# Kernel optimization log

Measured on AMD Instinct MI355X. Metric: run time of the kernel, lower is better.

The kernel has to match this reference:

```python
import jax, jax.numpy as jnp
import numpy as np

B, S, H, W, L = 32, 512, 768, 256, 8  # batch, subword seq, hidden, max words, max group size
INTENT, SLOT = 26, 121


def setup_inputs() -> dict:
    key = jax.random.key(0)
    ks = jax.random.split(key, 16)
    sc = 0.02
    res_all = jax.random.normal(ks[0], (B, S, H), jnp.float32)
    res = jax.random.normal(ks[1], (B, H), jnp.float32)
    # group covers indices start..start+lens inclusive (lens+1 <= L elements)
    token_start_idxs = jax.random.randint(ks[2], (B, W), 0, S - L, jnp.int32)
    subword_lengths = jax.random.randint(ks[3], (B, W), 1, L, jnp.int32)  # 1..7
    return {
        'res_all': res_all,
        'res': res,
        'token_start_idxs': token_start_idxs,
        'subword_lengths': subword_lengths,
        'Wsq_w': jax.random.normal(ks[4], (H, H), jnp.float32) * sc,
        'Wsq_b': jnp.zeros((H,), jnp.float32),
        'Wsk_w': jax.random.normal(ks[5], (H, H), jnp.float32) * sc,
        'Wsk_b': jnp.zeros((H,), jnp.float32),
        'Wsv_w': jax.random.normal(ks[6], (H, H), jnp.float32) * sc,
        'Wsv_b': jnp.zeros((H,), jnp.float32),
        'lin_id_w': jax.random.normal(ks[7], (INTENT, H), jnp.float32) * sc,
        'lin_id_b': jnp.zeros((INTENT,), jnp.float32),
        'lin_slot_w': jax.random.normal(ks[8], (SLOT, H), jnp.float32) * sc,
        'lin_slot_b': jnp.zeros((SLOT,), jnp.float32),
    }


def reference(res_all, res, token_start_idxs, subword_lengths,
              Wsq_w, Wsq_b, Wsk_w, Wsk_b, Wsv_w, Wsv_b,
              lin_id_w, lin_id_b, lin_slot_w, lin_slot_b):
    # intent head on pooled output
    res_id = res @ lin_id_w.T + lin_id_b  # [B, INTENT]

    # gather padded subword groups: torch.range is inclusive -> lens+1 subwords
    offs = jnp.arange(L, dtype=jnp.int32)                        # [L]
    idx = token_start_idxs[:, :, None] + offs[None, None, :]     # [B, W, L]
    idx = jnp.clip(idx, 0, S - 1)
    group = res_all[jnp.arange(B)[:, None, None], idx]           # [B, W, L, H]
    valid = offs[None, None, :] <= subword_lengths[:, :, None]   # [B, W, L], lens+1 valid

    # SAA_Attn: only the first row's attention output is used
    q0 = group[:, :, 0, :] @ Wsq_w.T + Wsq_b                     # [B, W, H]
    K = group @ Wsk_w.T + Wsk_b                                  # [B, W, L, H]
    V = group @ Wsv_w.T + Wsv_b                                  # [B, W, L, H]
    scores = jnp.einsum('bwh,bwkh->bwk', q0, K)                  # [B, W, L]
    scores = jnp.where(valid, scores, jnp.float32(-1e9))
    attn = jax.nn.softmax(scores, axis=-1)
    first = group[:, :, 0, :]
    attn_word = jnp.einsum('bwk,bwkh->bwh', attn, V) + first     # [B, W, H]

    # lens == 1 branch bypasses attention entirely
    word = jnp.where((subword_lengths == 1)[:, :, None], first, attn_word)

    res_sf = word @ lin_slot_w.T + lin_slot_b                    # [B, W, SLOT]
    return res_id, res_sf
```

## Files before the change

### kernel.cpp

```cpp
#include <hip/hip_runtime.h>
#include <cstdint>
#include <cstddef>

#define BB 32
#define SS 512
#define HH 768
#define WW 256
#define LL 8
#define NINTENT 26
#define NSLOT 121

typedef float f32x4 __attribute__((ext_vector_type(4)));
typedef __bf16 bf16x8 __attribute__((ext_vector_type(8)));

static __device__ __forceinline__ float bf2f(unsigned short u) {
    union { unsigned int i; float f; } x; x.i = ((unsigned int)u) << 16; return x.f;
}
static __device__ __forceinline__ unsigned short f2bf(float f) {
    union { float f; unsigned int i; } x; x.f = f;
    unsigned int r = (x.i + 0x7fffu + ((x.i >> 16) & 1u)) >> 16;
    return (unsigned short)r;
}

static __device__ __forceinline__ void gload16(const void* g, void* l) {
    __builtin_amdgcn_global_load_lds(
        (const __attribute__((address_space(1))) void*)g,
        (__attribute__((address_space(3))) void*)l, 16, 0, 0);
}

#define MF(a, b, c) __builtin_amdgcn_mfma_f32_16x16x32_bf16((a), (b), (c), 0, 0, 0)

__global__ __launch_bounds__(256) void prep_w(
    const float* __restrict__ Wk, const float* __restrict__ Wq,
    const float* __restrict__ Wv, const float* __restrict__ Ws,
    const float* __restrict__ bq, const float* __restrict__ bv,
    unsigned short* __restrict__ WkT_hi, unsigned short* __restrict__ WkT_lo,
    unsigned short* __restrict__ WqT_hi, unsigned short* __restrict__ WqT_lo,
    unsigned short* __restrict__ WvT, unsigned short* __restrict__ Wcomb,
    float* __restrict__ u_part,
    float* __restrict__ wsbv_part)
{
    int bid = blockIdx.x;
    int t = threadIdx.x;

    if (bid < 432) {
        __shared__ float tl[64][65];
        int mb = bid / 144, tb = bid % 144;
        int tx = tb % 12, ty = tb / 12;
        const float* src = (mb == 0) ? Wk : (mb == 1) ? Wq : Wv;
        int rr = t >> 4, c4 = (t & 15) * 4;
#pragma unroll
        for (int j = 0; j < 4; j++) {
            float4 v = *reinterpret_cast<const float4*>(
                &src[(size_t)(ty * 64 + rr + 16 * j) * HH + tx * 64 + c4]);
            tl[rr + 16 * j][c4 + 0] = v.x; tl[rr + 16 * j][c4 + 1] = v.y;
            tl[rr + 16 * j][c4 + 2] = v.z; tl[rr + 16 * j][c4 + 3] = v.w;
        }
        __syncthreads();
        int il = t >> 4, o4 = (t & 15) * 4;
        unsigned short* dhi = (mb == 0) ? WkT_hi : (mb == 1) ? WqT_hi : WvT;
        unsigned short* dlo = (mb == 0) ? WkT_lo : WqT_lo;
#pragma unroll
        for (int j = 0; j < 4; j++) {
            int i = il + 16 * j;
            float v0 = tl[o4 + 0][i], v1 = tl[o4 + 1][i];
            float v2 = tl[o4 + 2][i], v3 = tl[o4 + 3][i];
            size_t off = (size_t)(tx * 64 + i) * HH + ty * 64 + o4;
            ushort4 h;
            h.x = f2bf(v0); h.y = f2bf(v1); h.z = f2bf(v2); h.w = f2bf(v3);
            *reinterpret_cast<ushort4*>(&dhi[off]) = h;
            if (mb < 2) {
                ushort4 l;
                l.x = f2bf(v0 - bf2f(h.x)); l.y = f2bf(v1 - bf2f(h.y));
                l.z = f2bf(v2 - bf2f(h.z)); l.w = f2bf(v3 - bf2f(h.w));
                *reinterpret_cast<ushort4*>(&dlo[off]) = l;
            }
        }
        if (mb == 0) {
            int c = t >> 2, q = t & 3;
            float s = 0.f;
#pragma unroll
            for (int r = 0; r < 16; r++)
                s += bq[ty * 64 + q * 16 + r] * tl[q * 16 + r][c];
            s += __shfl_xor(s, 1);
            s += __shfl_xor(s, 2);
            if (q == 0) u_part[ty * HH + tx * 64 + c] = s;
        }
    } else {
        __shared__ float wred[4];
        int bid2 = bid - 432;
        int idx = bid2 * 256 + t;
        int row = idx / HH, col = idx % HH;
        float v = (row < NSLOT) ? Ws[row * HH + col] : 0.f;
        Wcomb[row * 1536 + col] = f2bf(v);
        float pv = v * bv[col];
        int lane = t & 63, wave = t >> 6;
#pragma unroll
        for (int off = 32; off > 0; off >>= 1) pv += __shfl_xor(pv, off);
        if (lane == 0) wred[wave] = pv;
        __syncthreads();
        if (t == 0)
            wsbv_part[(bid2 % 3) * 128 + row] = wred[0] + wred[1] + wred[2] + wred[3];
    }
}

__global__ __launch_bounds__(256) void gemm_weights(
    const uint4* __restrict__ WkT_hi, const uint4* __restrict__ WkT_lo,
    const uint4* __restrict__ WqT_hi, const uint4* __restrict__ WqT_lo,
    const uint4* __restrict__ WvT, const uint4* __restrict__ Wcomb,
    const float* __restrict__ res_all, const int* __restrict__ starts,
    const float* __restrict__ res, const float* __restrict__ id_w,
    const float* __restrict__ id_b,
    float* __restrict__ Ppart,
    float* __restrict__ WRpart,
    unsigned short* __restrict__ slotA,
    float* __restrict__ out)
{
    __shared__ uint4 sA[512];
    __shared__ uint4 sB[512];
    int bid = blockIdx.x;
    int t = threadIdx.x;
    int lane = t & 63, wave = t >> 6;

    if (bid >= 2384) {
        int w = (bid - 2384) * 4 + wave;
        int bb = w / 26, o = w - bb * 26;
        const float* rrow = res + bb * HH + lane * 12;
        const float* wrow = id_w + o * HH + lane * 12;
        float s = 0.f;
#pragma unroll
        for (int c = 0; c < 3; c++) {
            float4 a = *reinterpret_cast<const float4*>(&rrow[c * 4]);
            float4 b = *reinterpret_cast<const float4*>(&wrow[c * 4]);
            s += a.x * b.x + a.y * b.y + a.z * b.z + a.w * b.w;
        }
#pragma unroll
        for (int off = 32; off > 0; off >>= 1) s += __shfl_xor(s, off);
        if (lane == 0) out[bb * NINTENT + o] = s + id_b[o];
        return;
    }
    if (bid >= 336) {
        int gw = (bid - 336) * 4 + wave;
        int b = gw >> 8;
        int s0 = starts[gw];
        const float* src = res_all + (size_t)(b * SS + s0) * HH + lane * 12;
        unsigned short* dst = slotA + (size_t)gw * 1536 + lane * 12;
#pragma unroll
        for (int c2 = 0; c2 < 3; c2++) {
            float4 v = *reinterpret_cast<const float4*>(&src[c2 * 4]);
            ushort4 o;
            o.x = f2bf(v.x); o.y = f2bf(v.y); o.z = f2bf(v.z); o.w = f2bf(v.w);
            *reinterpret_cast<ushort4*>(&dst[c2 * 4]) = o;
        }
        return;
    }

    int wm = wave >> 1, wn = wave & 1;
    int l16 = lane & 15, lk = lane >> 4;
    int srow = lane >> 2, schk = lane & 3;
    uint4* sA0 = &sA[wave * 128];
    uint4* sA1 = &sA[wave * 128 + 64];
    uint4* sB0 = &sB[wave * 128];
    uint4* sB1 = &sB[wave * 128 + 64];

    f32x4 acc[4][4] = {};

    if (bid < 288) {
        int tile = bid >> 3, ks = bid & 7;
        int mt = tile / 6, nt = tile % 6;
        int kb = ks * 12;
#pragma unroll
        for (int p = 0; p < 3; p++) {
            const uint4* Ab = (p == 1) ? WkT_lo : WkT_hi;
            const uint4* Bb = (p == 2) ? WqT_lo : WqT_hi;
            const uint4* Ag0 = Ab + (size_t)(mt * 128 + wave * 32 + srow) * 96 + kb + schk;
            const uint4* Ag1 = Ag0 + (size_t)16 * 96;
            const uint4* Bg0 = Bb + (size_t)(nt * 128 + wave * 32 + srow) * 96 + kb + schk;
            const uint4* Bg1 = Bg0 + (size_t)16 * 96;
            for (int k0 = 0; k0 < 12; k0 += 4) {
                gload16(Ag0 + k0, sA0); gload16(Ag1 + k0, sA1);
                gload16(Bg0 + k0, sB0); gload16(Bg1 + k0, sB1);
                __syncthreads();
                bf16x8 af[4], bfr[4];
#pragma unroll
                for (int i = 0; i < 4; i++)
                    af[i] = *reinterpret_cast<const bf16x8*>(&sA[(wm * 64 + i * 16 + l16) * 4 + lk]);
#pragma unroll
                for (int j = 0; j < 4; j++)
                    bfr[j] = *reinterpret_cast<const bf16x8*>(&sB[(wn * 64 + j * 16 + l16) * 4 + lk]);
#pragma unroll
                for (int i = 0; i < 4; i++)
#pragma unroll
                    for (int j = 0; j < 4; j++)
                        acc[i][j] = MF(af[i], bfr[j], acc[i][j]);
                __syncthreads();
            }
        }
        float* dst = Ppart + (size_t)ks * 589824;
#pragma unroll
        for (int i = 0; i < 4; i++)
#pragma unroll
            for (int j = 0; j < 4; j++) {
                int col = nt * 128 + wn * 64 + j * 16 + l16;
#pragma unroll
                for (int q = 0; q < 4; q++) {
                    int row = mt * 128 + wm * 64 + i * 16 + lk * 4 + q;
                    dst[(size_t)row * HH + col] = acc[i][j][q];
                }
            }
    } else {
        int idx = bid - 288;
        int nt = idx >> 3, ks = idx & 7;
        int kb = ks * 12;
        const uint4* Ag0 = Wcomb + (size_t)(wave * 32 + srow) * 192 + kb + schk;
        const uint4* Ag1 = Ag0 + (size_t)16 * 192;
        const uint4* Bg0 = WvT + (size_t)(nt * 128 + wave * 32 + srow) * 96 + kb + schk;
        const uint4* Bg1 = Bg0 + (size_t)16 * 96;
        for (int k0 = 0; k0 < 12; k0 += 4) {
            gload16(Ag0 + k0, sA0); gload16(Ag1 + k0, sA1);
            gload16(Bg0 + k0, sB0); gload16(Bg1 + k0, sB1);
            __syncthreads();
            bf16x8 af[4], bfr[4];
#pragma unroll
            for (int i = 0; i < 4; i++)
                af[i] = *reinterpret_cast<const bf16x8*>(&sA[(wm * 64 + i * 16 + l16) * 4 + lk]);
#pragma unroll
            for (int j = 0; j < 4; j++)
                bfr[j] = *reinterpret_cast<const bf16x8*>(&sB[(wn * 64 + j * 16 + l16) * 4 + lk]);
#pragma unroll
            for (int i = 0; i < 4; i++)
#pragma unroll
                for (int j = 0; j < 4; j++)
                    acc[i][j] = MF(af[i], bfr[j], acc[i][j]);
            __syncthreads();
        }
        float* dst = WRpart + (size_t)ks * 98304;
#pragma unroll
        for (int i = 0; i < 4; i++)
#pragma unroll
            for (int j = 0; j < 4; j++) {
                int col = nt * 128 + wn * 64 + j * 16 + l16;
#pragma unroll
                for (int q = 0; q < 4; q++) {
                    int row = wm * 64 + i * 16 + lk * 4 + q;
                    dst[(size_t)row * HH + col] = acc[i][j][q];
                }
            }
    }
}

__global__ __launch_bounds__(256) void psum_kernel(
    const float4* __restrict__ Ppart, ushort4* __restrict__ Pb,
    const float4* __restrict__ WRpart, unsigned short* __restrict__ Wcomb,
    const float* __restrict__ u_part, float* __restrict__ u,
    const float* __restrict__ wsbv_part, float* __restrict__ wsbv)
{
    int bid = blockIdx.x, t = threadIdx.x;
    if (bid < 576) {
        int i = bid * 256 + t;
        float4 s = Ppart[i];
#pragma unroll
        for (int k = 1; k < 8; k++) {
            float4 v = Ppart[(size_t)k * 147456 + i];
            s.x += v.x; s.y += v.y; s.z += v.z; s.w += v.w;
        }
        ushort4 o;
        o.x = f2bf(s.x); o.y = f2bf(s.y); o.z = f2bf(s.z); o.w = f2bf(s.w);
        Pb[i] = o;
    } else if (bid < 672) {
        int q = (bid - 576) * 256 + t;
        float4 s = WRpart[q];
#pragma unroll
        for (int k = 1; k < 8; k++) {
            float4 v = WRpart[(size_t)k * 24576 + q];
            s.x += v.x; s.y += v.y; s.z += v.z; s.w += v.w;
        }
        int row = q / 192, colq = q % 192;
        ushort4 o;
        o.x = f2bf(s.x); o.y = f2bf(s.y); o.z = f2bf(s.z); o.w = f2bf(s.w);
        *reinterpret_cast<ushort4*>(&Wcomb[row * 1536 + 768 + colq * 4]) = o;
    } else if (bid < 675) {
        int c = (bid - 672) * 256 + t;
        float s = 0.f;
#pragma unroll
        for (int ty = 0; ty < 12; ty++) s += u_part[ty * HH + c];
        u[c] = s;
    } else if (t < 128) {
        wsbv[t] = wsbv_part[t] + wsbv_part[128 + t] + wsbv_part[256 + t];
    }
}

__global__ __launch_bounds__(256) void gemm_qp_sl(
    const uint4* __restrict__ A,
    const uint4* __restrict__ Bm,
    const uint4* __restrict__ Wc,
    const float* __restrict__ u,
    unsigned short* __restrict__ qp,
    float* __restrict__ Cpart0)
{
    __shared__ uint4 sA[256];
    __shared__ uint4 sB[512];

    int bid = blockIdx.x;
    int t = threadIdx.x;
    int lane = t & 63, wave = t >> 6;
    int wm = wave >> 1, wn = wave & 1;
    int l16 = lane & 15, lk = lane >> 4;
    int srow = lane >> 2, schk = lane & 3;

    if (bid >= 768) {
        int mt = bid - 768;
        const uint4* Ag  = A + (size_t)(mt * 32 + wave * 16 + srow) * 192 + schk;
        const uint4* Bg0 = Wc + (size_t)(wave * 32 + srow) * 192 + schk;
        const uint4* Bg1 = Bg0 + (size_t)16 * 192;
        uint4* sB0 = &sB[wave * 128];
        uint4* sB1 = &sB[wave * 128 + 64];

        f32x4 acc[4] = {};
        for (int k0 = 0; k0 < 96; k0 += 4) {
            if (wave < 2) gload16(Ag + k0, &sA[wave * 64]);
            gload16(Bg0 + k0, sB0);
            gload16(Bg1 + k0, sB1);
            __syncthreads();
            bf16x8 af = *reinterpret_cast<const bf16x8*>(&sA[(wm * 16 + l16) * 4 + lk]);
            bf16x8 bfr[4];
#pragma unroll
            for (int j = 0; j < 4; j++)
                bfr[j] = *reinterpret_cast<const bf16x8*>(&sB[(wn * 64 + j * 16 + l16) * 4 + lk]);
#pragma unroll
            for (int j = 0; j < 4; j++)
                acc[j] = MF(af, bfr[j], acc[j]);
            __syncthreads();
        }
#pragma unroll
        for (int j = 0; j < 4; j++) {
            int col = wn * 64 + j * 16 + l16;
#pragma unroll
            for (int q = 0; q < 4; q++) {
                int row = mt * 32 + wm * 16 + lk * 4 + q;
                Cpart0[(size_t)row * 128 + col] = acc[j][q];
            }
        }
        return;
    }

    bid = (bid & 7) * 96 + (bid >> 3);
    int mt = bid / 6, nt = bid % 6;

    const uint4* Ag  = A + (size_t)(mt * 64 + wave * 16 + srow) * 192 + schk;
    const uint4* Bg0 = Bm + (size_t)(nt * 128 + wave * 32 + srow) * 96 + schk;
    const uint4* Bg1 = Bg0 + (size_t)16 * 96;
    uint4* sAp = &sA[wave * 64];
    uint4* sB0 = &sB[wave * 128];
    uint4* sB1 = &sB[wave * 128 + 64];

    f32x4 acc[2][4] = {};

    for (int k0 = 0; k0 < 96; k0 += 4) {
        gload16(Ag + k0, sAp);
        gload16(Bg0 + k0, sB0);
        gload16(Bg1 + k0, sB1);
        __syncthreads();
        bf16x8 af[2], bfr[4];
#pragma unroll
        for (int i = 0; i < 2; i++)
            af[i] = *reinterpret_cast<const bf16x8*>(&sA[(wm * 32 + i * 16 + l16) * 4 + lk]);
#pragma unroll
        for (int j = 0; j < 4; j++)
            bfr[j] = *reinterpret_cast<const bf16x8*>(&sB[(wn * 64 + j * 16 + l16) * 4 + lk]);
#pragma unroll
        for (int i = 0; i < 2; i++)
#pragma unroll
            for (int j = 0; j < 4; j++)
                acc[i][j] = MF(af[i], bfr[j], acc[i][j]);
        __syncthreads();
    }

#pragma unroll
    for (int i = 0; i < 2; i++)
#pragma unroll
        for (int j = 0; j < 4; j++) {
            int col = nt * 128 + wn * 64 + j * 16 + l16;
            float add = u[col];
#pragma unroll
            for (int q = 0; q < 4; q++) {
                int row = mt * 64 + wm * 32 + i * 16 + lk * 4 + q;
                qp[(size_t)row * HH + col] = f2bf(acc[i][j][q] + add);
            }
        }
}

__global__ __launch_bounds__(256) void attn2_kernel(
    const unsigned short* __restrict__ qp,
    const float* __restrict__ res_all,
    const int* __restrict__ starts,
    const int* __restrict__ lens,
    unsigned short* __restrict__ slotA)
{
    int bid = blockIdx.x;
    bid = (bid & 7) * 256 + (bid >> 3);
    int gw = bid * 4 + (threadIdx.x >> 6);
    int lane = threadIdx.x & 63;
    int b = gw >> 8;
    int s0 = starts[gw];
    int sl = lens[gw];

    unsigned short* dst = slotA + (size_t)gw * 1536 + 768 + lane * 12;

    if (sl == 1) {
        ushort4 z = {0, 0, 0, 0};
#pragma unroll
        for (int c = 0; c < 3; c++) *reinterpret_cast<ushort4*>(&dst[c * 4]) = z;
        return;
    }

    const unsigned short* qrow = qp + (size_t)gw * HH + lane * 12;
    float q[12];
#pragma unroll
    for (int c = 0; c < 3; c++) {
        ushort4 v = *reinterpret_cast<const ushort4*>(&qrow[c * 4]);
        q[c * 4 + 0] = bf2f(v.x); q[c * 4 + 1] = bf2f(v.y);
        q[c * 4 + 2] = bf2f(v.z); q[c * 4 + 3] = bf2f(v.w);
    }

    float m = -1e30f, ssum = 0.f;
    float acc[12];
#pragma unroll
    for (int i = 0; i < 12; i++) acc[i] = 0.f;

    for (int k = 0; k < LL; k++) {
        if (k > sl) break;
        int s = s0 + k; if (s > SS - 1) s = SS - 1;
        const float* xr = res_all + (size_t)(b * SS + s) * HH + lane * 12;
        float x[12];
        float partial = 0.f;
#pragma unroll
        for (int c = 0; c < 3; c++) {
            float4 v = *reinterpret_cast<const float4*>(&xr[c * 4]);
            x[c * 4 + 0] = v.x; x[c * 4 + 1] = v.y;
            x[c * 4 + 2] = v.z; x[c * 4 + 3] = v.w;
            partial += q[c * 4 + 0] * v.x + q[c * 4 + 1] * v.y
                     + q[c * 4 + 2] * v.z + q[c * 4 + 3] * v.w;
        }
#pragma unroll
        for (int off = 32; off > 0; off >>= 1) partial += __shfl_xor(partial, off);

        float mnew = (partial > m) ? partial : m;
        float scale = __expf(m - mnew);
        float e = __expf(partial - mnew);
        ssum = ssum * scale + e;
#pragma unroll
        for (int i = 0; i < 12; i++) acc[i] = acc[i] * scale + e * x[i];
        m = mnew;
    }

    float inv = 1.f / ssum;
#pragma unroll
    for (int c = 0; c < 3; c++) {
        ushort4 o;
        o.x = f2bf(acc[c * 4 + 0] * inv); o.y = f2bf(acc[c * 4 + 1] * inv);
        o.z = f2bf(acc[c * 4 + 2] * inv); o.w = f2bf(acc[c * 4 + 3] * inv);
        *reinterpret_cast<ushort4*>(&dst[c * 4]) = o;
    }
}

__global__ __launch_bounds__(256) void gemm_slot_r(
    const uint4* __restrict__ A,
    const uint4* __restrict__ Bm,
    const float* __restrict__ Cpart0,
    const float* __restrict__ bias, const float* __restrict__ wsbv,
    const int* __restrict__ lens,
    float* __restrict__ outsf)
{
    __shared__ uint4 sA[128];
    __shared__ uint4 sB[512];

    int mt = blockIdx.x;
    int t = threadIdx.x;
    int lane = t & 63, wave = t >> 6;
    int wm = wave >> 1, wn = wave & 1;
    int l16 = lane & 15, lk = lane >> 4;
    int srow = lane >> 2, schk = lane & 3;

    const uint4* Ag  = A + (size_t)(mt * 32 + wave * 16 + srow) * 192 + 96 + schk;
    const uint4* Bg0 = Bm + (size_t)(wave * 32 + srow) * 192 + 96 + schk;
    const uint4* Bg1 = Bg0 + (size_t)16 * 192;
    uint4* sB0 = &sB[wave * 128];
    uint4* sB1 = &sB[wave * 128 + 64];

    f32x4 acc[4] = {};

    for (int k0 = 0; k0 < 96; k0 += 4) {
        if (wave < 2) gload16(Ag + k0, &sA[wave * 64]);
        gload16(Bg0 + k0, sB0);
        gload16(Bg1 + k0, sB1);
        __syncthreads();
        bf16x8 af = *reinterpret_cast<const bf16x8*>(&sA[(wm * 16 + l16) * 4 + lk]);
        bf16x8 bfr[4];
#pragma unroll
        for (int j = 0; j < 4; j++)
            bfr[j] = *reinterpret_cast<const bf16x8*>(&sB[(wn * 64 + j * 16 + l16) * 4 + lk]);
#pragma unroll
        for (int j = 0; j < 4; j++)
            acc[j] = MF(af, bfr[j], acc[j]);
        __syncthreads();
    }

#pragma unroll
    for (int j = 0; j < 4; j++) {
        int col = wn * 64 + j * 16 + l16;
        if (col < NSLOT) {
            float bc = bias[col], wv = wsbv[col];
#pragma unroll
            for (int q = 0; q < 4; q++) {
                int row = mt * 32 + wm * 16 + lk * 4 + q;
                float v = acc[j][q] + Cpart0[(size_t)row * 128 + col]
                        + bc + ((lens[row] > 1) ? wv : 0.f);
                outsf[(size_t)row * NSLOT + col] = v;
            }
        }
    }
}

extern "C" void kernel_launch(void* const* d_in, const int* in_sizes, int n_in,
                              void* d_out, int out_size, void* d_ws, size_t ws_size,
                              hipStream_t stream) {
    const float* res_all    = (const float*)d_in[0];
    const float* res        = (const float*)d_in[1];
    const int*   starts     = (const int*)d_in[2];
    const int*   lens       = (const int*)d_in[3];
    const float* Wsq_w      = (const float*)d_in[4];
    const float* Wsq_b      = (const float*)d_in[5];
    const float* Wsk_w      = (const float*)d_in[6];
    const float* Wsk_b      = (const float*)d_in[7];
    const float* Wsv_w      = (const float*)d_in[8];
    const float* Wsv_b      = (const float*)d_in[9];
    const float* lin_id_w   = (const float*)d_in[10];
    const float* lin_id_b   = (const float*)d_in[11];
    const float* lin_slot_w = (const float*)d_in[12];
    const float* lin_slot_b = (const float*)d_in[13];
    float* out = (float*)d_out;
    (void)Wsk_b;

    char* ws = (char*)d_ws;
    unsigned short* slotA     = (unsigned short*)(ws + 0);
    unsigned short* qp        = (unsigned short*)(ws + 25165824);
    unsigned short* WkT_hi    = (unsigned short*)(ws + 50331648);
    unsigned short* WkT_lo    = (unsigned short*)(ws + 51511296);
    unsigned short* WqT_hi    = (unsigned short*)(ws + 52690944);
    unsigned short* WqT_lo    = (unsigned short*)(ws + 53870592);
    unsigned short* WvT       = (unsigned short*)(ws + 55050240);
    unsigned short* Pb        = (unsigned short*)(ws + 56229888);
    unsigned short* Wcomb     = (unsigned short*)(ws + 57409536);
    float*          u         = (float*)(ws + 57802752);
    float*          wsbv      = (float*)(ws + 57805824);
    float*          u_part    = (float*)(ws + 57806336);
    float*          wsbv_part = (float*)(ws + 57843200);
    float*          Ppart     = (float*)(ws + 57845760);
    float*          WRpart    = (float*)(ws + 76720128);
    float*          Cpart0    = (float*)(ws + 79865856);

    prep_w<<<816, 256, 0, stream>>>(
        Wsk_w, Wsq_w, Wsv_w, lin_slot_w, Wsq_b, Wsv_b,
        WkT_hi, WkT_lo, WqT_hi, WqT_lo, WvT, Wcomb,
        u_part, wsbv_part);

    gemm_weights<<<2592, 256, 0, stream>>>(
        (const uint4*)WkT_hi, (const uint4*)WkT_lo,
        (const uint4*)WqT_hi, (const uint4*)WqT_lo,
        (const uint4*)WvT, (const uint4*)Wcomb,
        res_all, starts, res, lin_id_w, lin_id_b,
        Ppart, WRpart, slotA, out);

    psum_kernel<<<676, 256, 0, stream>>>(
        (const float4*)Ppart, (ushort4*)Pb, (const float4*)WRpart, Wcomb,
        u_part, u, wsbv_part, wsbv);

    gemm_qp_sl<<<1024, 256, 0, stream>>>((const uint4*)slotA, (const uint4*)Pb,
                                         (const uint4*)Wcomb, u, qp, Cpart0);

    attn2_kernel<<<2048, 256, 0, stream>>>(qp, res_all, starts, lens, slotA);

    gemm_slot_r<<<256, 256, 0, stream>>>((const uint4*)slotA, (const uint4*)Wcomb,
                                         Cpart0, lin_slot_b, wsbv, lens, out + 832);
}
```

Baseline: 86.44 us.

## Replace split-K partial buffers and reduction kernel with atomic accumulation

Split-K partial results for the weight-product GEMMs are now accumulated with float atomicAdd into zero-initialised buffers, which are cleared by extra blocks in the prep kernel. This removes the separate psum reduction kernel and its 8-way partial-buffer traffic. The u and wsbv reductions move into spare blocks of gemm_weights. Downstream GEMMs now read the fp32 accumulators and convert them to bf16 while staging into LDS, in place of async global-to-LDS loads of prepacked bf16. The cost is atomic contention, nondeterministic summation order, and more expensive B-operand staging in gemm_qp_sl and gemm_slot_r.

```diff
diff --git a/kernel.cpp b/kernel.cpp
--- a/kernel.cpp
+++ b/kernel.cpp
@@ -26,6 +26,17 @@
     __builtin_amdgcn_global_load_lds(
         (const __attribute__((address_space(1))) void*)g,
         (__attribute__((address_space(3))) void*)l, 16, 0, 0);
+}
+
+static __device__ __forceinline__ void stage_f32_bf16(const float* g, uint4* dst) {
+    float4 v0 = *reinterpret_cast<const float4*>(g);
+    float4 v1 = *reinterpret_cast<const float4*>(g + 4);
+    union { ushort4 h[2]; uint4 u; } pk;
+    pk.h[0].x = f2bf(v0.x); pk.h[0].y = f2bf(v0.y);
+    pk.h[0].z = f2bf(v0.z); pk.h[0].w = f2bf(v0.w);
+    pk.h[1].x = f2bf(v1.x); pk.h[1].y = f2bf(v1.y);
+    pk.h[1].z = f2bf(v1.z); pk.h[1].w = f2bf(v1.w);
+    *dst = pk.u;
 }
 
 #define MF(a, b, c) __builtin_amdgcn_mfma_f32_16x16x32_bf16((a), (b), (c), 0, 0, 0)
@@ -38,7 +49,9 @@
     unsigned short* __restrict__ WqT_hi, unsigned short* __restrict__ WqT_lo,
     unsigned short* __restrict__ WvT, unsigned short* __restrict__ Wcomb,
     float* __restrict__ u_part,
-    float* __restrict__ wsbv_part)
+    float* __restrict__ wsbv_part,
+    float* __restrict__ Pacc,
+    float* __restrict__ WRacc)
 {
     int bid = blockIdx.x;
     int t = threadIdx.x;
@@ -86,7 +99,7 @@
             s += __shfl_xor(s, 2);
             if (q == 0) u_part[ty * HH + tx * 64 + c] = s;
         }
-    } else {
+    } else if (bid < 816) {
         __shared__ float wred[4];
         int bid2 = bid - 432;
         int idx = bid2 * 256 + t;
@@ -101,6 +114,11 @@
         __syncthreads();
         if (t == 0)
             wsbv_part[(bid2 % 3) * 128 + row] = wred[0] + wred[1] + wred[2] + wred[3];
+    } else {
+        float4 z = {0.f, 0.f, 0.f, 0.f};
+        int zb = bid - 816;
+        if (zb < 576) ((float4*)Pacc)[zb * 256 + t] = z;
+        else          ((float4*)WRacc)[(zb - 576) * 256 + t] = z;
     }
 }
 
@@ -111,8 +129,10 @@
     const float* __restrict__ res_all, const int* __restrict__ starts,
     const float* __restrict__ res, const float* __restrict__ id_w,
     const float* __restrict__ id_b,
-    float* __restrict__ Ppart,
-    float* __restrict__ WRpart,
+    const float* __restrict__ u_part, const float* __restrict__ wsbv_part,
+    float* __restrict__ Pacc,
+    float* __restrict__ WRacc,
+    float* __restrict__ u, float* __restrict__ wsbv,
     unsigned short* __restrict__ slotA,
     float* __restrict__ out)
 {
@@ -122,6 +142,18 @@
     int t = threadIdx.x;
     int lane = t & 63, wave = t >> 6;
 
+    if (bid >= 2592) {
+        if (bid < 2595) {
+            int c = (bid - 2592) * 256 + t;
+            float s = 0.f;
+#pragma unroll
+            for (int ty = 0; ty < 12; ty++) s += u_part[ty * HH + c];
+            u[c] = s;
+        } else if (t < 128) {
+            wsbv[t] = wsbv_part[t] + wsbv_part[128 + t] + wsbv_part[256 + t];
+        }
+        return;
+    }
     if (bid >= 2384) {
         int w = (bid - 2384) * 4 + wave;
         int bb = w / 26, o = w - bb * 26;
@@ -196,7 +228,6 @@
                 __syncthreads();
             }
         }
-        float* dst = Ppart + (size_t)ks * 589824;
 #pragma unroll
         for (int i = 0; i < 4; i++)
 #pragma unroll
@@ -205,7 +236,7 @@
 #pragma unroll
                 for (int q = 0; q < 4; q++) {
                     int row = mt * 128 + wm * 64 + i * 16 + lk * 4 + q;
-                    dst[(size_t)row * HH + col] = acc[i][j][q];
+                    atomicAdd(&Pacc[(size_t)row * HH + col], acc[i][j][q]);
                 }
             }
     } else {
@@ -234,7 +265,6 @@
                     acc[i][j] = MF(af[i], bfr[j], acc[i][j]);
             __syncthreads();
         }
-        float* dst = WRpart + (size_t)ks * 98304;
 #pragma unroll
         for (int i = 0; i < 4; i++)
 #pragma unroll
@@ -243,56 +273,15 @@
 #pragma unroll
                 for (int q = 0; q < 4; q++) {
                     int row = wm * 64 + i * 16 + lk * 4 + q;
-                    dst[(size_t)row * HH + col] = acc[i][j][q];
+                    atomicAdd(&WRacc[(size_t)row * HH + col], acc[i][j][q]);
                 }
             }
-    }
-}
-
-__global__ __launch_bounds__(256) void psum_kernel(
-    const float4* __restrict__ Ppart, ushort4* __restrict__ Pb,
-    const float4* __restrict__ WRpart, unsigned short* __restrict__ Wcomb,
-    const float* __restrict__ u_part, float* __restrict__ u,
-    const float* __restrict__ wsbv_part, float* __restrict__ wsbv)
-{
-    int bid = blockIdx.x, t = threadIdx.x;
-    if (bid < 576) {
-        int i = bid * 256 + t;
-        float4 s = Ppart[i];
-#pragma unroll
-        for (int k = 1; k < 8; k++) {
-            float4 v = Ppart[(size_t)k * 147456 + i];
-            s.x += v.x; s.y += v.y; s.z += v.z; s.w += v.w;
-        }
-        ushort4 o;
-        o.x = f2bf(s.x); o.y = f2bf(s.y); o.z = f2bf(s.z); o.w = f2bf(s.w);
-        Pb[i] = o;
-    } else if (bid < 672) {
-        int q = (bid - 576) * 256 + t;
-        float4 s = WRpart[q];
-#pragma unroll
-        for (int k = 1; k < 8; k++) {
-            float4 v = WRpart[(size_t)k * 24576 + q];
-            s.x += v.x; s.y += v.y; s.z += v.z; s.w += v.w;
-        }
-        int row = q / 192, colq = q % 192;
-        ushort4 o;
-        o.x = f2bf(s.x); o.y = f2bf(s.y); o.z = f2bf(s.z); o.w = f2bf(s.w);
-        *reinterpret_cast<ushort4*>(&Wcomb[row * 1536 + 768 + colq * 4]) = o;
-    } else if (bid < 675) {
-        int c = (bid - 672) * 256 + t;
-        float s = 0.f;
-#pragma unroll
-        for (int ty = 0; ty < 12; ty++) s += u_part[ty * HH + c];
-        u[c] = s;
-    } else if (t < 128) {
-        wsbv[t] = wsbv_part[t] + wsbv_part[128 + t] + wsbv_part[256 + t];
     }
 }
 
 __global__ __launch_bounds__(256) void gemm_qp_sl(
     const uint4* __restrict__ A,
-    const uint4* __restrict__ Bm,
+    const float* __restrict__ Pacc,
     const uint4* __restrict__ Wc,
     const float* __restrict__ u,
     unsigned short* __restrict__ qp,
@@ -347,9 +336,9 @@
     bid = (bid & 7) * 96 + (bid >> 3);
     int mt = bid / 6, nt = bid % 6;
 
-    const uint4* Ag  = A + (size_t)(mt * 64 + wave * 16 + srow) * 192 + schk;
-    const uint4* Bg0 = Bm + (size_t)(nt * 128 + wave * 32 + srow) * 96 + schk;
-    const uint4* Bg1 = Bg0 + (size_t)16 * 96;
+    const uint4* Ag = A + (size_t)(mt * 64 + wave * 16 + srow) * 192 + schk;
+    const float* Bf0 = Pacc + (size_t)(nt * 128 + wave * 32 + srow) * HH + schk * 8;
+    const float* Bf1 = Bf0 + (size_t)16 * HH;
     uint4* sAp = &sA[wave * 64];
     uint4* sB0 = &sB[wave * 128];
     uint4* sB1 = &sB[wave * 128 + 64];
@@ -358,8 +347,8 @@
 
     for (int k0 = 0; k0 < 96; k0 += 4) {
         gload16(Ag + k0, sAp);
-        gload16(Bg0 + k0, sB0);
-        gload16(Bg1 + k0, sB1);
+        stage_f32_bf16(Bf0 + (size_t)k0 * 8, &sB0[lane]);
+        stage_f32_bf16(Bf1 + (size_t)k0 * 8, &sB1[lane]);
         __syncthreads();
         bf16x8 af[2], bfr[4];
 #pragma unroll
@@ -466,7 +455,7 @@
 
 __global__ __launch_bounds__(256) void gemm_slot_r(
     const uint4* __restrict__ A,
-    const uint4* __restrict__ Bm,
+    const float* __restrict__ WRacc,
     const float* __restrict__ Cpart0,
     const float* __restrict__ bias, const float* __restrict__ wsbv,
     const int* __restrict__ lens,
@@ -482,9 +471,9 @@
     int l16 = lane & 15, lk = lane >> 4;
     int srow = lane >> 2, schk = lane & 3;
 
-    const uint4* Ag  = A + (size_t)(mt * 32 + wave * 16 + srow) * 192 + 96 + schk;
-    const uint4* Bg0 = Bm + (size_t)(wave * 32 + srow) * 192 + 96 + schk;
-    const uint4* Bg1 = Bg0 + (size_t)16 * 192;
+    const uint4* Ag = A + (size_t)(mt * 32 + wave * 16 + srow) * 192 + 96 + schk;
+    const float* Bf0 = WRacc + (size_t)(wave * 32 + srow) * HH + schk * 8;
+    const float* Bf1 = Bf0 + (size_t)16 * HH;
     uint4* sB0 = &sB[wave * 128];
     uint4* sB1 = &sB[wave * 128 + 64];
 
@@ -492,8 +481,8 @@
 
     for (int k0 = 0; k0 < 96; k0 += 4) {
         if (wave < 2) gload16(Ag + k0, &sA[wave * 64]);
-        gload16(Bg0 + k0, sB0);
-        gload16(Bg1 + k0, sB1);
+        stage_f32_bf16(Bf0 + (size_t)k0 * 8, &sB0[lane]);
+        stage_f32_bf16(Bf1 + (size_t)k0 * 8, &sB1[lane]);
         __syncthreads();
         bf16x8 af = *reinterpret_cast<const bf16x8*>(&sA[(wm * 16 + l16) * 4 + lk]);
         bf16x8 bfr[4];
@@ -550,37 +539,32 @@
     unsigned short* WqT_hi    = (unsigned short*)(ws + 52690944);
     unsigned short* WqT_lo    = (unsigned short*)(ws + 53870592);
     unsigned short* WvT       = (unsigned short*)(ws + 55050240);
-    unsigned short* Pb        = (unsigned short*)(ws + 56229888);
     unsigned short* Wcomb     = (unsigned short*)(ws + 57409536);
     float*          u         = (float*)(ws + 57802752);
     float*          wsbv      = (float*)(ws + 57805824);
     float*          u_part    = (float*)(ws + 57806336);
     float*          wsbv_part = (float*)(ws + 57843200);
-    float*          Ppart     = (float*)(ws + 57845760);
-    float*          WRpart    = (float*)(ws + 76720128);
-    float*          Cpart0    = (float*)(ws + 79865856);
-
-    prep_w<<<816, 256, 0, stream>>>(
+    float*          Pacc      = (float*)(ws + 57845760);
+    float*          WRacc     = (float*)(ws + 60205056);
+    float*          Cpart0    = (float*)(ws + 60598272);
+
+    prep_w<<<1488, 256, 0, stream>>>(
         Wsk_w, Wsq_w, Wsv_w, lin_slot_w, Wsq_b, Wsv_b,
         WkT_hi, WkT_lo, WqT_hi, WqT_lo, WvT, Wcomb,
-        u_part, wsbv_part);
-
-    gemm_weights<<<2592, 256, 0, stream>>>(
+        u_part, wsbv_part, Pacc, WRacc);
+
+    gemm_weights<<<2596, 256, 0, stream>>>(
         (const uint4*)WkT_hi, (const uint4*)WkT_lo,
         (const uint4*)WqT_hi, (const uint4*)WqT_lo,
         (const uint4*)WvT, (const uint4*)Wcomb,
         res_all, starts, res, lin_id_w, lin_id_b,
-        Ppart, WRpart, slotA, out);
-
-    psum_kernel<<<676, 256, 0, stream>>>(
-        (const float4*)Ppart, (ushort4*)Pb, (const float4*)WRpart, Wcomb,
-        u_part, u, wsbv_part, wsbv);
-
-    gemm_qp_sl<<<1024, 256, 0, stream>>>((const uint4*)slotA, (const uint4*)Pb,
+        u_part, wsbv_part, Pacc, WRacc, u, wsbv, slotA, out);
+
+    gemm_qp_sl<<<1024, 256, 0, stream>>>((const uint4*)slotA, Pacc,
                                          (const uint4*)Wcomb, u, qp, Cpart0);
 
     attn2_kernel<<<2048, 256, 0, stream>>>(qp, res_all, starts, lens, slotA);
 
-    gemm_slot_r<<<256, 256, 0, stream>>>((const uint4*)slotA, (const uint4*)Wcomb,
+    gemm_slot_r<<<256, 256, 0, stream>>>((const uint4*)slotA, WRacc,
                                          Cpart0, lin_slot_b, wsbv, lens, out + 832);
 }
```

Result: slower. 101.1 us (+17.0%).
